# Performance work log

Measured on AMD Instinct MI355X. Metric: run time of the kernel, lower is better.

The kernel has to match this reference:

```python
import jax, jax.numpy as jnp
import numpy as np

D_MODEL = 1024
N_HEADS = 16
HEAD_DIM = D_MODEL // N_HEADS
D_FF = 4 * D_MODEL


def _layernorm(x, g, b, eps=1e-5):
    mu = jnp.mean(x, axis=-1, keepdims=True)
    var = jnp.var(x, axis=-1, keepdims=True)
    return (x - mu) * jax.lax.rsqrt(var + eps) * g + b


def setup_inputs() -> dict:
    key = jax.random.key(0)
    ks = jax.random.split(key, 12)
    s = lambda fan_in: 1.0 / np.sqrt(fan_in)
    x = jax.random.normal(ks[0], (2, 2048, D_MODEL), dtype=jnp.float32)
    return {
        "x": x,
        "ln1_g": jnp.ones((D_MODEL,), jnp.float32),
        "ln1_b": jnp.zeros((D_MODEL,), jnp.float32),
        "w_qkv": jax.random.uniform(ks[1], (D_MODEL, 3 * D_MODEL), jnp.float32, -s(D_MODEL), s(D_MODEL)),
        "b_qkv": jax.random.uniform(ks[2], (3 * D_MODEL,), jnp.float32, -s(D_MODEL), s(D_MODEL)),
        "w_out": jax.random.uniform(ks[3], (D_MODEL, D_MODEL), jnp.float32, -s(D_MODEL), s(D_MODEL)),
        "b_out": jax.random.uniform(ks[4], (D_MODEL,), jnp.float32, -s(D_MODEL), s(D_MODEL)),
        "ln2_g": jnp.ones((D_MODEL,), jnp.float32),
        "ln2_b": jnp.zeros((D_MODEL,), jnp.float32),
        "w_ff1": jax.random.uniform(ks[5], (D_MODEL, D_FF), jnp.float32, -s(D_MODEL), s(D_MODEL)),
        "b_ff1": jax.random.uniform(ks[6], (D_FF,), jnp.float32, -s(D_MODEL), s(D_MODEL)),
        "w_ff2": jax.random.uniform(ks[7], (D_FF, D_MODEL), jnp.float32, -s(D_FF), s(D_FF)),
        "b_ff2": jax.random.uniform(ks[8], (D_MODEL,), jnp.float32, -s(D_FF), s(D_FF)),
    }


def reference(x, ln1_g, ln1_b, w_qkv, b_qkv, w_out, b_out,
              ln2_g, ln2_b, w_ff1, b_ff1, w_ff2, b_ff2):
    B, T, C = x.shape
    # --- pre-LN causal self-attention + residual ---
    h = _layernorm(x, ln1_g, ln1_b)
    qkv = h @ w_qkv + b_qkv                                  # [B,T,3C]
    qkv = qkv.reshape(B, T, 3, N_HEADS, HEAD_DIM)
    q, k, v = qkv[:, :, 0], qkv[:, :, 1], qkv[:, :, 2]       # [B,T,H,Dh]
    scores = jnp.einsum("bthd,bshd->bhts", q, k) / np.sqrt(HEAD_DIM).astype(np.float32)
    causal = jnp.tril(jnp.ones((T, T), dtype=bool))
    scores = jnp.where(causal, scores, -jnp.inf)
    weights = jax.nn.softmax(scores, axis=-1)                # [B,H,T,T]
    attn = jnp.einsum("bhts,bshd->bthd", weights, v).reshape(B, T, C)
    x = x + attn @ w_out + b_out
    # --- pre-LN GELU FFN + residual ---
    h = _layernorm(x, ln2_g, ln2_b)
    h = jax.nn.gelu(h @ w_ff1 + b_ff1, approximate=False)    # torch GELU = erf
    x = x + h @ w_ff2 + b_ff2
    return x
```

## Files before the change

kernel.cpp:

```cpp
#include <hip/hip_runtime.h>
#include <hip/hip_bf16.h>
#include <math.h>

#define TSEQ 2048
#define BATCH 2
#define CDIM 1024
#define NH 16
#define HD 64
#define DFF 4096
#define ROWS (BATCH*TSEQ)

typedef __attribute__((ext_vector_type(4))) float f32x4;
typedef __attribute__((ext_vector_type(8))) short bf16x8;
typedef __attribute__((ext_vector_type(4))) unsigned short u16x4;

__device__ __forceinline__ void gload_lds16(const void* g, void* l) {
    void* gv = const_cast<void*>(g);
    __builtin_amdgcn_global_load_lds((__attribute__((address_space(1))) void*)gv,
                                     (__attribute__((address_space(3))) void*)l, 16, 0, 0);
}

__device__ __forceinline__ unsigned short f2bf(float f) {
    unsigned int u = __float_as_uint(f);
    return (unsigned short)((u + 0x7FFFu + ((u >> 16) & 1u)) >> 16);
}
__device__ __forceinline__ float bf2f(unsigned short u) {
    return __uint_as_float((unsigned int)u << 16);
}
__device__ __forceinline__ unsigned int cvt_pk_bf16(float lo, float hi) {
    unsigned int r;
    asm("v_cvt_pk_bf16_f32 %0, %1, %2" : "=v"(r) : "v"(lo), "v"(hi));
    return r;
}
__device__ __forceinline__ float fast_gelu(float v) {
    float u = fmaf(0.044715f * v * v, v, v);
    float e = __expf(-1.5957691216057308f * u);
    return v * __builtin_amdgcn_rcpf(1.0f + e);
}

__global__ __launch_bounds__(256) void ln_kernel(const float* __restrict__ x,
                                                 const float* __restrict__ g,
                                                 const float* __restrict__ b,
                                                 unsigned short* __restrict__ out) {
    int row = blockIdx.x;
    int tid = threadIdx.x;
    const float* xr = x + (size_t)row * CDIM;
    float4 v = *(const float4*)(xr + tid * 4);
    float s  = v.x + v.y + v.z + v.w;
    float s2 = v.x*v.x + v.y*v.y + v.z*v.z + v.w*v.w;
    #pragma unroll
    for (int off = 32; off >= 1; off >>= 1) {
        s  += __shfl_down(s, off);
        s2 += __shfl_down(s2, off);
    }
    __shared__ float red[8];
    int wid = tid >> 6, lane = tid & 63;
    if (lane == 0) { red[wid] = s; red[wid + 4] = s2; }
    __syncthreads();
    float ts  = red[0] + red[1] + red[2] + red[3];
    float ts2 = red[4] + red[5] + red[6] + red[7];
    float mu  = ts * (1.0f / CDIM);
    float var = ts2 * (1.0f / CDIM) - mu * mu;
    float rstd = rsqrtf(var + 1e-5f);
    float4 gv = *(const float4*)(g + tid * 4);
    float4 bv = *(const float4*)(b + tid * 4);
    unsigned short o4[4];
    o4[0] = f2bf((v.x - mu) * rstd * gv.x + bv.x);
    o4[1] = f2bf((v.y - mu) * rstd * gv.y + bv.y);
    o4[2] = f2bf((v.z - mu) * rstd * gv.z + bv.z);
    o4[3] = f2bf((v.w - mu) * rstd * gv.w + bv.w);
    *(u16x4*)(out + (size_t)row * CDIM + tid * 4) = *(u16x4*)o4;
}

__global__ __launch_bounds__(256) void prep_kernel(
        const float* __restrict__ w_qkv, const float* __restrict__ w_out,
        const float* __restrict__ w_ff1, const float* __restrict__ w_ff2,
        const float* __restrict__ x, const float* __restrict__ ln1_g,
        const float* __restrict__ ln1_b,
        unsigned short* __restrict__ wqkvT, unsigned short* __restrict__ woutT,
        unsigned short* __restrict__ wff1T, unsigned short* __restrict__ wff2T,
        unsigned short* __restrict__ h_bf) {
    __shared__ float T[64][65];
    __shared__ float red[8];
    int bid = blockIdx.x;
    int tid = threadIdx.x;

    if (bid >= 3072) {
        const int row = bid - 3072;
        const float* xr = x + (size_t)row * CDIM;
        float4 v = *(const float4*)(xr + tid * 4);
        float s  = v.x + v.y + v.z + v.w;
        float s2 = v.x*v.x + v.y*v.y + v.z*v.z + v.w*v.w;
        #pragma unroll
        for (int off = 32; off >= 1; off >>= 1) {
            s  += __shfl_down(s, off);
            s2 += __shfl_down(s2, off);
        }
        int wid = tid >> 6, lane = tid & 63;
        if (lane == 0) { red[wid] = s; red[wid + 4] = s2; }
        __syncthreads();
        float ts  = red[0] + red[1] + red[2] + red[3];
        float ts2 = red[4] + red[5] + red[6] + red[7];
        float mu  = ts * (1.0f / CDIM);
        float var = ts2 * (1.0f / CDIM) - mu * mu;
        float rstd = rsqrtf(var + 1e-5f);
        float4 gv = *(const float4*)(ln1_g + tid * 4);
        float4 bv = *(const float4*)(ln1_b + tid * 4);
        unsigned short o4[4];
        o4[0] = f2bf((v.x - mu) * rstd * gv.x + bv.x);
        o4[1] = f2bf((v.y - mu) * rstd * gv.y + bv.y);
        o4[2] = f2bf((v.z - mu) * rstd * gv.z + bv.z);
        o4[3] = f2bf((v.w - mu) * rstd * gv.w + bv.w);
        *(u16x4*)(h_bf + (size_t)row * CDIM + tid * 4) = *(u16x4*)o4;
        return;
    }

    const float* W; unsigned short* Wt; int K, N, nbx;
    if (bid < 768)       {             W = w_qkv; Wt = wqkvT; K = 1024; N = 3072; nbx = 48; }
    else if (bid < 1024) { bid -= 768;  W = w_out; Wt = woutT; K = 1024; N = 1024; nbx = 16; }
    else if (bid < 2048) { bid -= 1024; W = w_ff1; Wt = wff1T; K = 1024; N = 4096; nbx = 64; }
    else                 { bid -= 2048; W = w_ff2; Wt = wff2T; K = 4096; N = 1024; nbx = 16; }
    const int n0 = (bid % nbx) * 64, k0 = (bid / nbx) * 64;

    int kr = tid >> 4;
    int nc = (tid & 15) * 4;
    #pragma unroll
    for (int i = 0; i < 4; ++i) {
        float4 v = *(const float4*)&W[(size_t)(k0 + kr + i*16) * N + (n0 + nc)];
        T[kr + i*16][nc + 0] = v.x;
        T[kr + i*16][nc + 1] = v.y;
        T[kr + i*16][nc + 2] = v.z;
        T[kr + i*16][nc + 3] = v.w;
    }
    __syncthreads();
    int n  = tid >> 2;
    int kb = (tid & 3) * 16;
    unsigned short tmp[16];
    #pragma unroll
    for (int i = 0; i < 16; ++i) tmp[i] = f2bf(T[kb + i][n]);
    unsigned short* dst = Wt + (size_t)(n0 + n) * K + (k0 + kb);
    *(int4*)dst       = *(int4*)&tmp[0];
    *(int4*)(dst + 8) = *(int4*)&tmp[8];
}

template<int EPI>
__global__ __launch_bounds__(512) void gemm_kernel(const unsigned short* __restrict__ A,
                                                   const unsigned short* __restrict__ Bt,
                                                   const float* __restrict__ bias,
                                                   const float* __restrict__ res,
                                                   void* __restrict__ Cout,
                                                   unsigned short* __restrict__ kfrag_,
                                                   unsigned short* __restrict__ vfrag_,
                                                   int M, int N, int K,
                                                   int nxc, int xcw, int xrw) {
    __shared__ __align__(16) unsigned short As[3 * 8192];
    __shared__ __align__(16) unsigned short Bs[3 * 8192];
    const int tid = threadIdx.x;
    const int l   = tid & 63;
    const int w   = tid >> 6;
    const int wr  = (w >> 2) * 128;
    const int wcl = (w & 3) * 64;
    const int lin = blockIdx.x;
    const int xcd = lin & 7;
    const int idx = lin >> 3;
    const int xc  = xcd % nxc, xr = xcd / nxc;
    const long brow = (long)(xr * xrw + idx / xcw) * 256;
    const long bcol = (long)(xc * xcw + idx % xcw) * 256;

    const int srow = tid >> 2;
    const int schk = ((tid & 3) ^ ((srow >> 1) & 3)) * 8;
    const unsigned short* gA = A  + (size_t)(brow + srow) * K + schk;
    const unsigned short* gB = Bt + (size_t)(bcol + srow) * K + schk;

    f32x4 acc[8][4];
    #pragma unroll
    for (int m = 0; m < 8; ++m)
        #pragma unroll
        for (int n = 0; n < 4; ++n) acc[m][n] = (f32x4){0.f, 0.f, 0.f, 0.f};

    #define STAGE256(buf, koff_)                                                       \
        do {                                                                           \
            unsigned short* lA_ = As + (buf) * 8192 + tid * 8;                         \
            unsigned short* lB_ = Bs + (buf) * 8192 + tid * 8;                         \
            gload_lds16(gA + (koff_), lA_);                                            \
            gload_lds16(gA + (size_t)128 * K + (koff_), lA_ + 4096);                   \
            gload_lds16(gB + (koff_), lB_);                                            \
            gload_lds16(gB + (size_t)128 * K + (koff_), lB_ + 4096);                   \
        } while (0)

    STAGE256(0, 0);
    STAGE256(1, 32);

    int cur = 0;
    for (int k0 = 0; k0 < K; k0 += 32) {
        if (k0 + 32 < K) asm volatile("s_waitcnt vmcnt(4)" ::: "memory");
        else             asm volatile("s_waitcnt vmcnt(0)" ::: "memory");
        __builtin_amdgcn_s_barrier();
        asm volatile("" ::: "memory");

        const unsigned short* cA = As + cur * 8192;
        const unsigned short* cB = Bs + cur * 8192;
        const int koff = ((l >> 4) ^ (((l & 15) >> 1) & 3)) * 8;
        bf16x8 af[8], bf[4];
        #pragma unroll
        for (int m = 0; m < 8; ++m)
            af[m] = *(const bf16x8*)&cA[(wr + m * 16 + (l & 15)) * 32 + koff];
        #pragma unroll
        for (int n = 0; n < 4; ++n)
            bf[n] = *(const bf16x8*)&cB[(wcl + n * 16 + (l & 15)) * 32 + koff];
        __builtin_amdgcn_s_setprio(1);
        #pragma unroll
        for (int m = 0; m < 8; ++m)
            #pragma unroll
            for (int n = 0; n < 4; ++n)
                acc[m][n] = __builtin_amdgcn_mfma_f32_16x16x32_bf16(af[m], bf[n], acc[m][n], 0, 0, 0);
        __builtin_amdgcn_s_setprio(0);

        if (k0 + 64 < K) {
            int nxt = cur + 2; if (nxt >= 3) nxt -= 3;
            STAGE256(nxt, k0 + 64);
        }
        cur = cur + 1; if (cur == 3) cur = 0;
    }
    #undef STAGE256

    const int reg = (int)(bcol >> 10);
    #pragma unroll
    for (int m = 0; m < 8; ++m) {
        const int rown = wr + m * 16 + (l >> 4) * 4;
        #pragma unroll
        for (int n = 0; n < 4; ++n) {
            const long col = bcol + wcl + n * 16 + (l & 15);
            const float bb = bias[col];
            #pragma unroll
            for (int r = 0; r < 4; ++r) {
                const long row = brow + rown + r;
                float v = acc[m][n][r] + bb;
                if (EPI == 1) {
                    v += res[row * N + col];
                    ((float*)Cout)[row * N + col] = v;
                } else if (EPI == 2) {
                    ((unsigned short*)Cout)[row * N + col] = f2bf(fast_gelu(v));
                } else if (EPI == 3) {
                    const unsigned short bv = f2bf(v);
                    if (reg == 0) {
                        ((unsigned short*)Cout)[row * 1024 + col] = bv;
                    } else {
                        const int dfull = (int)col - reg * 1024;
                        const int hh = dfull >> 6, dd = dfull & 63;
                        const int bb2 = (int)(row >> 11), tt = (int)(row & 2047);
                        const int jj = tt >> 6;
                        const size_t tb = ((size_t)((bb2 * 16 + hh) * 32 + jj)) * 8;
                        if (reg == 1) {
                            const int sb2 = (tt >> 4) & 3, llo = tt & 15;
                            const int gg2 = dd >> 5, lhi = (dd >> 3) & 3, ii = dd & 7;
                            kfrag_[(tb + sb2 * 2 + gg2) * 512 + (lhi * 16 + llo) * 8 + ii] = bv;
                        } else {
                            const int kb2 = (tt >> 5) & 1, lhi = (tt >> 3) & 3, ii = tt & 7;
                            const int db2 = dd >> 4, llo = dd & 15;
                            vfrag_[(tb + kb2 * 4 + db2) * 512 + (lhi * 16 + llo) * 8 + ii] = bv;
                        }
                    }
                } else {
                    ((unsigned short*)Cout)[row * N + col] = f2bf(v);
                }
            }
        }
    }
}

template<int EPI>
__global__ __launch_bounds__(512) void gemm128x8_kernel(const unsigned short* __restrict__ A,
                                                        const unsigned short* __restrict__ Bt,
                                                        const float* __restrict__ bias,
                                                        const float* __restrict__ res,
                                                        void* __restrict__ Cout,
                                                        int M, int N, int K,
                                                        int nxc, int xcw, int xrw) {
    __shared__ __align__(16) unsigned short As[3 * 8192];
    __shared__ __align__(16) unsigned short Bs[3 * 8192];
    const int tid = threadIdx.x;
    const int l   = tid & 63;
    const int w   = tid >> 6;
    const int wr  = (w >> 1) * 32;
    const int wc  = (w & 1) * 64;
    const int lin = blockIdx.x;
    const int xcd = lin & 7;
    const int idx = lin >> 3;
    const int xc  = xcd % nxc, xr = xcd / nxc;
    const long brow = (long)(xr * xrw + idx / xcw) * 128;
    const long bcol = (long)(xc * xcw + idx % xcw) * 128;

    const int srow = tid >> 3;
    const int schk = ((tid & 7) ^ (srow & 7)) * 8;
    const unsigned short* gA = A  + (size_t)(brow + srow) * K + schk;
    const unsigned short* gB = Bt + (size_t)(bcol + srow) * K + schk;

    f32x4 acc[2][4];
    #pragma unroll
    for (int m = 0; m < 2; ++m)
        #pragma unroll
        for (int n = 0; n < 4; ++n) acc[m][n] = (f32x4){0.f, 0.f, 0.f, 0.f};

    #define STAGE128W8(buf, koff_)                                                     \
        do {                                                                           \
            unsigned short* lA_ = As + (buf) * 8192 + tid * 8;                         \
            unsigned short* lB_ = Bs + (buf) * 8192 + tid * 8;                         \
            gload_lds16(gA + (koff_), lA_);                                            \
            gload_lds16(gA + (size_t)64 * K + (koff_), lA_ + 4096);                    \
            gload_lds16(gB + (koff_), lB_);                                            \
            gload_lds16(gB + (size_t)64 * K + (koff_), lB_ + 4096);                    \
        } while (0)

    STAGE128W8(0, 0);
    STAGE128W8(1, 64);

    int cur = 0;
    for (int k0 = 0; k0 < K; k0 += 64) {
        if (k0 + 64 < K) asm volatile("s_waitcnt vmcnt(4)" ::: "memory");
        else             asm volatile("s_waitcnt vmcnt(0)" ::: "memory");
        __builtin_amdgcn_s_barrier();
        asm volatile("" ::: "memory");

        const unsigned short* cA = As + cur * 8192;
        const unsigned short* cB = Bs + cur * 8192;
        #pragma unroll
        for (int gg = 0; gg < 2; ++gg) {
            const int koff = ((gg * 4 + (l >> 4)) ^ (l & 7)) * 8;
            bf16x8 af[2], bf[4];
            #pragma unroll
            for (int m = 0; m < 2; ++m)
                af[m] = *(const bf16x8*)&cA[(wr + m * 16 + (l & 15)) * 64 + koff];
            #pragma unroll
            for (int n = 0; n < 4; ++n)
                bf[n] = *(const bf16x8*)&cB[(wc + n * 16 + (l & 15)) * 64 + koff];
            __builtin_amdgcn_s_setprio(1);
            #pragma unroll
            for (int m = 0; m < 2; ++m)
                #pragma unroll
                for (int n = 0; n < 4; ++n)
                    acc[m][n] = __builtin_amdgcn_mfma_f32_16x16x32_bf16(af[m], bf[n], acc[m][n], 0, 0, 0);
            __builtin_amdgcn_s_setprio(0);
        }

        if (k0 + 128 < K) {
            int nxt = cur + 2; if (nxt >= 3) nxt -= 3;
            STAGE128W8(nxt, k0 + 128);
        }
        cur = cur + 1; if (cur == 3) cur = 0;
    }
    #undef STAGE128W8

    #pragma unroll
    for (int m = 0; m < 2; ++m) {
        const int rown = wr + m * 16 + (l >> 4) * 4;
        #pragma unroll
        for (int n = 0; n < 4; ++n) {
            const long col = bcol + wc + n * 16 + (l & 15);
            const float bb = bias[col];
            #pragma unroll
            for (int r = 0; r < 4; ++r) {
                const long row = brow + rown + r;
                float v = acc[m][n][r] + bb;
                if (EPI == 1) {
                    v += res[row * N + col];
                    ((float*)Cout)[row * N + col] = v;
                } else if (EPI == 2) {
                    ((unsigned short*)Cout)[row * N + col] = f2bf(fast_gelu(v));
                } else {
                    ((unsigned short*)Cout)[row * N + col] = f2bf(v);
                }
            }
        }
    }
}

#define QSCALE 0.18033688011112042f
#define RTHR 8.0f
__global__ __launch_bounds__(64) void attn_kernel(const unsigned short* __restrict__ qbuf,
                                                  const unsigned short* __restrict__ kfrag,
                                                  const unsigned short* __restrict__ vfrag,
                                                  unsigned short* __restrict__ out) {
    __shared__ __align__(16) unsigned short Ps[16 * 128];

    const int l    = threadIdx.x;
    const int q    = l & 15;
    const int g    = l >> 4;
    const int lin  = blockIdx.x;
    const int xcd  = lin & 7;
    const int rest = lin >> 3;
    const int h    = xcd + 8 * (rest & 1);
    const int b    = (rest >> 1) & 1;
    const int strip = 127 - (rest >> 2);
    const int jmax  = strip >> 2;
    const size_t rowbase = (size_t)b * TSEQ;
    const int bh = b * NH + h;
    const int qglob = strip * 16 + q;

    const unsigned short* kfb = kfrag + (size_t)bh * 32 * 8 * 512;
    const unsigned short* vfb = vfrag + (size_t)bh * 32 * 8 * 512;

    bf16x8 aq0, aq1;
    {
        const unsigned short* qp = qbuf + (rowbase + qglob) * 1024 + h * 64 + g * 8;
        bf16x8 t0 = *(const bf16x8*)qp;
        bf16x8 t1 = *(const bf16x8*)(qp + 32);
        #pragma unroll
        for (int i = 0; i < 8; ++i) {
            aq0[i] = (short)f2bf(bf2f((unsigned short)t0[i]) * QSCALE);
            aq1[i] = (short)f2bf(bf2f((unsigned short)t1[i]) * QSCALE);
        }
    }

    float mrow = -INFINITY, lrow = 0.f;
    f32x4 o[4];
    #pragma unroll
    for (int d = 0; d < 4; ++d) o[d] = (f32x4){0.f, 0.f, 0.f, 0.f};

    for (int j = 0; j + 1 <= jmax; j += 2) {
        const bool diag2 = (j + 1 == jmax);

        bf16x8 kf[16];
        #pragma unroll
        for (int t = 0; t < 2; ++t)
            #pragma unroll
            for (int sb = 0; sb < 4; ++sb) {
                const unsigned short* kp = kfb + (size_t)((j + t) * 8 + sb * 2) * 512 + l * 8;
                kf[t * 8 + sb * 2]     = *(const bf16x8*)kp;
                kf[t * 8 + sb * 2 + 1] = *(const bf16x8*)(kp + 512);
            }

        f32x4 sf[8];
        __builtin_amdgcn_s_setprio(1);
        #pragma unroll
        for (int t = 0; t < 2; ++t)
            #pragma unroll
            for (int sb = 0; sb < 4; ++sb) {
                f32x4 acc = (f32x4){0.f, 0.f, 0.f, 0.f};
                acc = __builtin_amdgcn_mfma_f32_16x16x32_bf16(kf[t*8 + sb*2],     aq0, acc, 0, 0, 0);
                acc = __builtin_amdgcn_mfma_f32_16x16x32_bf16(kf[t*8 + sb*2 + 1], aq1, acc, 0, 0, 0);
                sf[t*4 + sb] = acc;
            }
        __builtin_amdgcn_s_setprio(0);

        bf16x8 vf[16];
        #pragma unroll
        for (int kb = 0; kb < 4; ++kb)
            #pragma unroll
            for (int db = 0; db < 4; ++db)
                vf[kb * 4 + db] = *(const bf16x8*)(vfb + (size_t)((j + (kb >> 1)) * 8 + (kb & 1) * 4 + db) * 512 + l * 8);

        if (diag2) {
            #pragma unroll
            for (int sb = 0; sb < 4; ++sb) {
                const int sg = (j + 1) * 64 + sb * 16 + 4 * g;
                #pragma unroll
                for (int r = 0; r < 4; ++r)
                    if (sg + r > qglob) sf[4 + sb][r] = -INFINITY;
            }
        }

        f32x4 mv = sf[0];
        #pragma unroll
        for (int i = 1; i < 8; ++i)
            #pragma unroll
            for (int r = 0; r < 4; ++r) mv[r] = fmaxf(mv[r], sf[i][r]);
        float mloc = fmaxf(fmaxf(mv[0], mv[1]), fmaxf(mv[2], mv[3]));
        mloc = fmaxf(mloc, __shfl_xor(mloc, 16));
        mloc = fmaxf(mloc, __shfl_xor(mloc, 32));

        float mn;
        if (__all(mloc <= mrow + RTHR)) {
            mn = mrow;
        } else {
            mn = fmaxf(mrow, mloc);
            const float alpha = exp2f(mrow - mn);
            mrow = mn;
            lrow *= alpha;
            float al[4];
            #pragma unroll
            for (int r = 0; r < 4; ++r) al[r] = __shfl(alpha, g * 4 + r);
            #pragma unroll
            for (int d = 0; d < 4; ++d)
                #pragma unroll
                for (int r = 0; r < 4; ++r) o[d][r] *= al[r];
        }

        float psum = 0.f;
        #pragma unroll
        for (int i = 0; i < 8; ++i) {
            const int t = i >> 2, sb = i & 3;
            float p0 = exp2f(sf[i][0] - mn);
            float p1 = exp2f(sf[i][1] - mn);
            float p2 = exp2f(sf[i][2] - mn);
            float p3 = exp2f(sf[i][3] - mn);
            psum += (p0 + p1) + (p2 + p3);
            unsigned int pk0 = cvt_pk_bf16(p0, p1);
            unsigned int pk1 = cvt_pk_bf16(p2, p3);
            const int c16 = (t * 8 + sb * 2 + (g >> 1)) ^ (q & 7);
            *(uint2*)((char*)Ps + q * 256 + c16 * 16 + (g & 1) * 8) = make_uint2(pk0, pk1);
        }
        psum += __shfl_xor(psum, 16);
        psum += __shfl_xor(psum, 32);
        lrow += psum;

        __builtin_amdgcn_s_setprio(1);
        #pragma unroll
        for (int kb = 0; kb < 4; ++kb) {
            const int c16 = (kb * 4 + g) ^ (q & 7);
            bf16x8 pa = *(const bf16x8*)((const char*)Ps + q * 256 + c16 * 16);
            #pragma unroll
            for (int db = 0; db < 4; ++db)
                o[db] = __builtin_amdgcn_mfma_f32_16x16x32_bf16(pa, vf[kb * 4 + db], o[db], 0, 0, 0);
        }
        __builtin_amdgcn_s_setprio(0);
    }

    if ((jmax & 1) == 0) {
        const int j = jmax;
        bf16x8 kf[8];
        #pragma unroll
        for (int sb = 0; sb < 4; ++sb) {
            const unsigned short* kp = kfb + (size_t)(j * 8 + sb * 2) * 512 + l * 8;
            kf[sb * 2]     = *(const bf16x8*)kp;
            kf[sb * 2 + 1] = *(const bf16x8*)(kp + 512);
        }
        f32x4 sf[4];
        __builtin_amdgcn_s_setprio(1);
        #pragma unroll
        for (int sb = 0; sb < 4; ++sb) {
            f32x4 acc = (f32x4){0.f, 0.f, 0.f, 0.f};
            acc = __builtin_amdgcn_mfma_f32_16x16x32_bf16(kf[sb*2],     aq0, acc, 0, 0, 0);
            acc = __builtin_amdgcn_mfma_f32_16x16x32_bf16(kf[sb*2 + 1], aq1, acc, 0, 0, 0);
            sf[sb] = acc;
        }
        __builtin_amdgcn_s_setprio(0);

        bf16x8 vf[8];
        #pragma unroll
        for (int kb = 0; kb < 2; ++kb)
            #pragma unroll
            for (int db = 0; db < 4; ++db)
                vf[kb * 4 + db] = *(const bf16x8*)(vfb + (size_t)(j * 8 + kb * 4 + db) * 512 + l * 8);

        #pragma unroll
        for (int sb = 0; sb < 4; ++sb) {
            const int sg = j * 64 + sb * 16 + 4 * g;
            #pragma unroll
            for (int r = 0; r < 4; ++r)
                if (sg + r > qglob) sf[sb][r] = -INFINITY;
        }

        f32x4 mv = sf[0];
        #pragma unroll
        for (int i = 1; i < 4; ++i)
            #pragma unroll
            for (int r = 0; r < 4; ++r) mv[r] = fmaxf(mv[r], sf[i][r]);
        float mloc = fmaxf(fmaxf(mv[0], mv[1]), fmaxf(mv[2], mv[3]));
        mloc = fmaxf(mloc, __shfl_xor(mloc, 16));
        mloc = fmaxf(mloc, __shfl_xor(mloc, 32));

        float mn;
        if (__all(mloc <= mrow + RTHR)) {
            mn = mrow;
        } else {
            mn = fmaxf(mrow, mloc);
            const float alpha = exp2f(mrow - mn);
            mrow = mn;
            lrow *= alpha;
            float al[4];
            #pragma unroll
            for (int r = 0; r < 4; ++r) al[r] = __shfl(alpha, g * 4 + r);
            #pragma unroll
            for (int d = 0; d < 4; ++d)
                #pragma unroll
                for (int r = 0; r < 4; ++r) o[d][r] *= al[r];
        }

        float psum = 0.f;
        #pragma unroll
        for (int sb = 0; sb < 4; ++sb) {
            float p0 = exp2f(sf[sb][0] - mn);
            float p1 = exp2f(sf[sb][1] - mn);
            float p2 = exp2f(sf[sb][2] - mn);
            float p3 = exp2f(sf[sb][3] - mn);
            psum += (p0 + p1) + (p2 + p3);
            unsigned int pk0 = cvt_pk_bf16(p0, p1);
            unsigned int pk1 = cvt_pk_bf16(p2, p3);
            const int c16 = (sb * 2 + (g >> 1)) ^ (q & 7);
            *(uint2*)((char*)Ps + q * 256 + c16 * 16 + (g & 1) * 8) = make_uint2(pk0, pk1);
        }
        psum += __shfl_xor(psum, 16);
        psum += __shfl_xor(psum, 32);
        lrow += psum;

        __builtin_amdgcn_s_setprio(1);
        #pragma unroll
        for (int kb = 0; kb < 2; ++kb) {
            const int c16 = (kb * 4 + g) ^ (q & 7);
            bf16x8 pa = *(const bf16x8*)((const char*)Ps + q * 256 + c16 * 16);
            #pragma unroll
            for (int db = 0; db < 4; ++db)
                o[db] = __builtin_amdgcn_mfma_f32_16x16x32_bf16(pa, vf[kb * 4 + db], o[db], 0, 0, 0);
        }
        __builtin_amdgcn_s_setprio(0);
    }

    float linv[4];
    #pragma unroll
    for (int r = 0; r < 4; ++r) linv[r] = 1.0f / __shfl(lrow, g * 4 + r);
    #pragma unroll
    for (int r = 0; r < 4; ++r) {
        const size_t rb = (rowbase + strip * 16 + g * 4 + r) * (size_t)CDIM + h * 64 + q;
        #pragma unroll
        for (int d = 0; d < 4; ++d)
            out[rb + d * 16] = f2bf(o[d][r] * linv[r]);
    }
}

extern "C" void kernel_launch(void* const* d_in, const int* in_sizes, int n_in,
                              void* d_out, int out_size, void* d_ws, size_t ws_size,
                              hipStream_t stream) {
    const float* x     = (const float*)d_in[0];
    const float* ln1_g = (const float*)d_in[1];
    const float* ln1_b = (const float*)d_in[2];
    const float* w_qkv = (const float*)d_in[3];
    const float* b_qkv = (const float*)d_in[4];
    const float* w_out = (const float*)d_in[5];
    const float* b_out = (const float*)d_in[6];
    const float* ln2_g = (const float*)d_in[7];
    const float* ln2_b = (const float*)d_in[8];
    const float* w_ff1 = (const float*)d_in[9];
    const float* b_ff1 = (const float*)d_in[10];
    const float* w_ff2 = (const float*)d_in[11];
    const float* b_ff2 = (const float*)d_in[12];
    float* out = (float*)d_out;

    char* wsb = (char*)d_ws;
    unsigned short* h_bf    = (unsigned short*)(wsb);
    unsigned short* qbuf    = (unsigned short*)(wsb + 8ll  * 1024 * 1024);
    unsigned short* attn_bf = (unsigned short*)(wsb + 32ll * 1024 * 1024);
    float*          x1      = (float*)         (wsb + 40ll * 1024 * 1024);
    unsigned short* kfrag   = (unsigned short*)(wsb + 40ll * 1024 * 1024);
    unsigned short* vfrag   = (unsigned short*)(wsb + 48ll * 1024 * 1024);
    unsigned short* wqkvT   = (unsigned short*)(wsb + 56ll * 1024 * 1024);
    unsigned short* woutT   = (unsigned short*)(wsb + 62ll * 1024 * 1024);
    unsigned short* wff1T   = (unsigned short*)(wsb + 64ll * 1024 * 1024);
    unsigned short* wff2T   = (unsigned short*)(wsb + 72ll * 1024 * 1024);
    unsigned short* ff1_bf  = (unsigned short*)(wsb + 8ll  * 1024 * 1024);

    prep_kernel<<<7168, 256, 0, stream>>>(w_qkv, w_out, w_ff1, w_ff2,
                                          x, ln1_g, ln1_b,
                                          wqkvT, woutT, wff1T, wff2T, h_bf);
    gemm_kernel<3><<<192, 512, 0, stream>>>(h_bf, wqkvT, b_qkv, nullptr, qbuf,
                                            kfrag, vfrag, ROWS, 3072, 1024, 4, 3, 8);
    attn_kernel<<<4096, 64, 0, stream>>>(qbuf, kfrag, vfrag, attn_bf);
    gemm128x8_kernel<1><<<256, 512, 0, stream>>>(attn_bf, woutT, b_out, x, x1,
                                                 ROWS, 1024, 1024, 2, 4, 8);
    ln_kernel<<<ROWS, 256, 0, stream>>>(x1, ln2_g, ln2_b, h_bf);
    gemm_kernel<2><<<256, 512, 0, stream>>>(h_bf, wff1T, b_ff1, nullptr, ff1_bf,
                                            nullptr, nullptr, ROWS, 4096, 1024, 4, 4, 8);
    gemm128x8_kernel<1><<<256, 512, 0, stream>>>(ff1_bf, wff2T, b_ff2, x1, (float*)out,
                                                 ROWS, 1024, 4096, 2, 4, 8);
}
```

Before: 217.4 us.

## Split K across warp groups in 128x128 GEMM with LDS reduction

The 128x128 out-projection and FF2 GEMM is reorganized so that two groups of four waves each compute a full 64x64 sub-tile, handling alternate 64-wide K slices. At the end the partial sums are combined through shared memory before the bias and residual epilogue. Each wave now loads more A fragments per K step and issues 16 MFMAs instead of 8, which raises fragment reuse and cuts LDS reads per MFMA. The cost is that only half the waves issue MFMAs on any given K step, plus extra accumulator registers and a reduction pass at the end.

Result: no change. 214.8 us, median of 2 (-1.2%).

```diff
diff --git a/kernel.cpp b/kernel.cpp
--- a/kernel.cpp
+++ b/kernel.cpp
@@ -270,19 +270,21 @@
 }
 
 template<int EPI>
-__global__ __launch_bounds__(512) void gemm128x8_kernel(const unsigned short* __restrict__ A,
-                                                        const unsigned short* __restrict__ Bt,
-                                                        const float* __restrict__ bias,
-                                                        const float* __restrict__ res,
-                                                        void* __restrict__ Cout,
-                                                        int M, int N, int K,
-                                                        int nxc, int xcw, int xrw) {
-    __shared__ __align__(16) unsigned short As[3 * 8192];
-    __shared__ __align__(16) unsigned short Bs[3 * 8192];
+__global__ __launch_bounds__(512) void gemmsk_kernel(const unsigned short* __restrict__ A,
+                                                     const unsigned short* __restrict__ Bt,
+                                                     const float* __restrict__ bias,
+                                                     const float* __restrict__ res,
+                                                     void* __restrict__ Cout,
+                                                     int M, int N, int K,
+                                                     int nxc, int xcw, int xrw) {
+    __shared__ __align__(16) unsigned short smem[6 * 8192];
+    unsigned short* As = smem;
+    unsigned short* Bs = smem + 3 * 8192;
     const int tid = threadIdx.x;
     const int l   = tid & 63;
     const int w   = tid >> 6;
-    const int wr  = (w >> 1) * 32;
+    const int ks  = w >> 2;
+    const int wr  = ((w >> 1) & 1) * 64;
     const int wc  = (w & 1) * 64;
     const int lin = blockIdx.x;
     const int xcd = lin & 7;
@@ -296,13 +298,13 @@
     const unsigned short* gA = A  + (size_t)(brow + srow) * K + schk;
     const unsigned short* gB = Bt + (size_t)(bcol + srow) * K + schk;
 
-    f32x4 acc[2][4];
-    #pragma unroll
-    for (int m = 0; m < 2; ++m)
+    f32x4 acc[4][4];
+    #pragma unroll
+    for (int m = 0; m < 4; ++m)
         #pragma unroll
         for (int n = 0; n < 4; ++n) acc[m][n] = (f32x4){0.f, 0.f, 0.f, 0.f};
 
-    #define STAGE128W8(buf, koff_)                                                     \
+    #define STAGESK(buf, koff_)                                                        \
         do {                                                                           \
             unsigned short* lA_ = As + (buf) * 8192 + tid * 8;                         \
             unsigned short* lB_ = Bs + (buf) * 8192 + tid * 8;                         \
@@ -312,47 +314,70 @@
             gload_lds16(gB + (size_t)64 * K + (koff_), lB_ + 4096);                    \
         } while (0)
 
-    STAGE128W8(0, 0);
-    STAGE128W8(1, 64);
-
-    int cur = 0;
-    for (int k0 = 0; k0 < K; k0 += 64) {
+    STAGESK(0, 0);
+    STAGESK(1, 64);
+
+    int cur = 0, t = 0;
+    for (int k0 = 0; k0 < K; k0 += 64, ++t) {
         if (k0 + 64 < K) asm volatile("s_waitcnt vmcnt(4)" ::: "memory");
         else             asm volatile("s_waitcnt vmcnt(0)" ::: "memory");
         __builtin_amdgcn_s_barrier();
         asm volatile("" ::: "memory");
 
-        const unsigned short* cA = As + cur * 8192;
-        const unsigned short* cB = Bs + cur * 8192;
-        #pragma unroll
-        for (int gg = 0; gg < 2; ++gg) {
-            const int koff = ((gg * 4 + (l >> 4)) ^ (l & 7)) * 8;
-            bf16x8 af[2], bf[4];
-            #pragma unroll
-            for (int m = 0; m < 2; ++m)
-                af[m] = *(const bf16x8*)&cA[(wr + m * 16 + (l & 15)) * 64 + koff];
-            #pragma unroll
-            for (int n = 0; n < 4; ++n)
-                bf[n] = *(const bf16x8*)&cB[(wc + n * 16 + (l & 15)) * 64 + koff];
-            __builtin_amdgcn_s_setprio(1);
-            #pragma unroll
-            for (int m = 0; m < 2; ++m)
+        if ((t & 1) == ks) {
+            const unsigned short* cA = As + cur * 8192;
+            const unsigned short* cB = Bs + cur * 8192;
+            #pragma unroll
+            for (int gg = 0; gg < 2; ++gg) {
+                const int koff = ((gg * 4 + (l >> 4)) ^ (l & 7)) * 8;
+                bf16x8 af[4], bf[4];
+                #pragma unroll
+                for (int m = 0; m < 4; ++m)
+                    af[m] = *(const bf16x8*)&cA[(wr + m * 16 + (l & 15)) * 64 + koff];
                 #pragma unroll
                 for (int n = 0; n < 4; ++n)
-                    acc[m][n] = __builtin_amdgcn_mfma_f32_16x16x32_bf16(af[m], bf[n], acc[m][n], 0, 0, 0);
-            __builtin_amdgcn_s_setprio(0);
+                    bf[n] = *(const bf16x8*)&cB[(wc + n * 16 + (l & 15)) * 64 + koff];
+                __builtin_amdgcn_s_setprio(1);
+                #pragma unroll
+                for (int m = 0; m < 4; ++m)
+                    #pragma unroll
+                    for (int n = 0; n < 4; ++n)
+                        acc[m][n] = __builtin_amdgcn_mfma_f32_16x16x32_bf16(af[m], bf[n], acc[m][n], 0, 0, 0);
+                __builtin_amdgcn_s_setprio(0);
+            }
         }
 
         if (k0 + 128 < K) {
             int nxt = cur + 2; if (nxt >= 3) nxt -= 3;
-            STAGE128W8(nxt, k0 + 128);
+            STAGESK(nxt, k0 + 128);
         }
         cur = cur + 1; if (cur == 3) cur = 0;
     }
-    #undef STAGE128W8
-
-    #pragma unroll
-    for (int m = 0; m < 2; ++m) {
+    #undef STAGESK
+
+    __syncthreads();
+    float* red = (float*)smem;
+    const int rgn = w & 3;
+    if (ks == 1) {
+        #pragma unroll
+        for (int m = 0; m < 4; ++m)
+            #pragma unroll
+            for (int n = 0; n < 4; ++n)
+                *(f32x4*)&red[rgn * 4096 + l * 64 + ((m * 4 + n) ^ (l & 15)) * 4] = acc[m][n];
+    }
+    __syncthreads();
+    if (ks == 1) return;
+
+    #pragma unroll
+    for (int m = 0; m < 4; ++m)
+        #pragma unroll
+        for (int n = 0; n < 4; ++n) {
+            f32x4 p = *(const f32x4*)&red[rgn * 4096 + l * 64 + ((m * 4 + n) ^ (l & 15)) * 4];
+            acc[m][n] += p;
+        }
+
+    #pragma unroll
+    for (int m = 0; m < 4; ++m) {
         const int rown = wr + m * 16 + (l >> 4) * 4;
         #pragma unroll
         for (int n = 0; n < 4; ++n) {
@@ -655,11 +680,11 @@
     gemm_kernel<3><<<192, 512, 0, stream>>>(h_bf, wqkvT, b_qkv, nullptr, qbuf,
                                             kfrag, vfrag, ROWS, 3072, 1024, 4, 3, 8);
     attn_kernel<<<4096, 64, 0, stream>>>(qbuf, kfrag, vfrag, attn_bf);
-    gemm128x8_kernel<1><<<256, 512, 0, stream>>>(attn_bf, woutT, b_out, x, x1,
-                                                 ROWS, 1024, 1024, 2, 4, 8);
+    gemmsk_kernel<1><<<256, 512, 0, stream>>>(attn_bf, woutT, b_out, x, x1,
+                                              ROWS, 1024, 1024, 2, 4, 8);
     ln_kernel<<<ROWS, 256, 0, stream>>>(x1, ln2_g, ln2_b, h_bf);
     gemm_kernel<2><<<256, 512, 0, stream>>>(h_bf, wff1T, b_ff1, nullptr, ff1_bf,
                                             nullptr, nullptr, ROWS, 4096, 1024, 4, 4, 8);
-    gemm128x8_kernel<1><<<256, 512, 0, stream>>>(ff1_bf, wff2T, b_ff2, x1, (float*)out,
-                                                 ROWS, 1024, 4096, 2, 4, 8);
-}
+    gemmsk_kernel<1><<<256, 512, 0, stream>>>(ff1_bf, wff2T, b_ff2, x1, (float*)out,
+                                              ROWS, 1024, 4096, 2, 4, 8);
+}
```
